# Optimization experiments

Measured on AMD Instinct MI355X. Metric: run time of the kernel, lower is better.

The kernel has to match this reference:

```python
import jax, jax.numpy as jnp
import numpy as np

SIGMA = 0.1  # kernel-point influence radius (KPConv linear correlation)


def setup_inputs() -> dict:
    key = jax.random.key(0)
    k1, k2, k3, k4, k5 = jax.random.split(key, 5)
    N, K, KP, CIN, COUT = 65536, 32, 15, 64, 128
    pos = jax.random.uniform(k1, (N, 3), dtype=jnp.float32)
    feats = jax.random.normal(k2, (N, CIN), dtype=jnp.float32)
    kernel_points = jax.random.normal(k3, (KP, 3), dtype=jnp.float32) * 0.05
    weights = jax.random.normal(k4, (KP, CIN, COUT), dtype=jnp.float32) / np.sqrt(KP * CIN)
    neighbors = jax.random.randint(k5, (N, K), 0, N, dtype=jnp.int64)
    return {"pos": pos, "feats": feats, "kernel_points": kernel_points,
            "weights": weights, "neighbors": neighbors}


def reference(pos, feats, kernel_points, weights, neighbors):
    # pos: [N,3], feats: [N,Cin], kernel_points: [Kp,3],
    # weights: [Kp,Cin,Cout], neighbors: [N,K] int
    neigh_pos = pos[neighbors]                      # [N,K,3] irregular gather
    rel = neigh_pos - pos[:, None, :]               # [N,K,3]
    # distance from each relative neighbor offset to each kernel point
    d = rel[:, :, None, :] - kernel_points[None, None, :, :]   # [N,K,Kp,3]
    dist = jnp.sqrt(jnp.sum(d * d, axis=-1))        # [N,K,Kp]
    infl = jnp.maximum(0.0, 1.0 - dist / SIGMA)     # linear correlation
    neigh_feat = feats[neighbors]                   # [N,K,Cin] irregular gather
    # per-kernel-point weighted neighbor aggregation, then projection
    weighted = jnp.einsum('njk,njc->nkc', infl, neigh_feat)    # [N,Kp,Cin]
    out = jnp.einsum('nkc,kcd->nd', weighted, weights)         # [N,Cout]
    return out
```

## Files before the change

### kernel.cpp

```cpp
#include <hip/hip_runtime.h>

#define NPTS  65536
#define KNB   32
#define KPn   15
#define CIN   64
#define COUT  128
#define MPTS  16
#define THREADS 512
#define RCAP  96
#define CHUNK 32
#define ESTR  40
#define WSTR  1032
#define KSTEPS 32
#define NTILE 8
#define WELEMS (NTILE * KSTEPS * 64 * 8)

#define OFF_INFL   0
#define OFF_SFT    20480
#define ZERO_B16   ((20480 + 5120) / 16)
#define OFF_RLX    25600
#define OFF_RLY    (OFF_RLX + 384)
#define OFF_RLZ    (OFF_RLY + 384)
#define OFF_RLD    (OFF_RLZ + 384)
#define OFF_RSL    (OFF_RLD + 384)
#define POOL_BYTES (MPTS * WSTR * 2)

typedef __attribute__((ext_vector_type(8))) short short8;
typedef __attribute__((ext_vector_type(4))) float f32x4;

__device__ __forceinline__ unsigned int f2bf(float f) {
    union { float f; unsigned int i; } v; v.f = f;
    return (v.i + 0x7fffu + ((v.i >> 16) & 1u)) >> 16;
}
__device__ __forceinline__ unsigned int cvt_pk_bf16(float lo, float hi) {
    unsigned int r;
    asm volatile("v_cvt_pk_bf16_f32 %0, %1, %2" : "=v"(r) : "v"(lo), "v"(hi));
    return r;
}

__global__ void wtrans_kernel(const float* __restrict__ w,
                              const float* __restrict__ kpts,
                              unsigned short* __restrict__ wTf,
                              float4* __restrict__ kpq_out) {
    const int d = blockIdx.x * 256 + threadIdx.x;
    if (d < WELEMS) {
        const int j    = d & 7;
        const int lane = (d >> 3) & 63;
        const int ks   = (d >> 9) & 31;
        const int t    = d >> 14;
        const int f    = ks * 32 + ((lane >> 4) & 3) * 8 + j;
        const int k    = f & 15;
        const int c    = f >> 4;
        const int n    = t * 16 + (lane & 15);
        wTf[d] = (k < KPn)
            ? (unsigned short)f2bf(w[((size_t)k * CIN + c) * COUT + n])
            : (unsigned short)0;
    }
    if (blockIdx.x == 0 && threadIdx.x < 16) {
        const int k = threadIdx.x;
        if (k < KPn) {
            const float x = kpts[k * 3 + 0];
            const float y = kpts[k * 3 + 1];
            const float z = kpts[k * 3 + 2];
            kpq_out[k] = make_float4(x, y, z, x * x + y * y + z * z);
        } else {
            float mx = 0.f;
            for (int i = 0; i < KPn; ++i) {
                const float x = kpts[i * 3 + 0];
                const float y = kpts[i * 3 + 1];
                const float z = kpts[i * 3 + 2];
                mx = fmaxf(mx, x * x + y * y + z * z);
            }
            const float R = 0.1f + sqrtf(mx);
            kpq_out[15] = make_float4(R * R, 0.f, 0.f, 0.f);
        }
    }
}

__global__ __launch_bounds__(THREADS, 8) void kpconv_kernel(
    const float* __restrict__ pos,
    const float* __restrict__ feats,
    const unsigned short* __restrict__ wTf,
    const float4* __restrict__ kpq_in,
    const int*   __restrict__ neighbors,
    float*       __restrict__ out)
{
    __shared__ __align__(16) unsigned char pool[POOL_BYTES];
    __shared__ float  cposf[MPTS * 3];
    __shared__ float4 kpq[KPn];
    __shared__ int    nact;

    unsigned short* const wl     = (unsigned short*)pool;
    unsigned short* const infl   = (unsigned short*)(pool + OFF_INFL);
    unsigned short* const sfeatT = (unsigned short*)(pool + OFF_SFT);
    float*          const rlx    = (float*)(pool + OFF_RLX);
    float*          const rly    = (float*)(pool + OFF_RLY);
    float*          const rlz    = (float*)(pool + OFF_RLZ);
    float*          const rld    = (float*)(pool + OFF_RLD);
    unsigned int*   const rsl    = (unsigned int*)(pool + OFF_RSL);

    const int tid  = threadIdx.x;
    const int n0   = blockIdx.x * MPTS;
    const int lane = tid & 63;
    const int wv   = tid >> 6;
    const int m    = lane & 15;
    const int q    = lane >> 4;

    const int   p0  = tid >> 5;
    const int   nb0 = neighbors[(size_t)n0 * KNB + tid];
    const float qx  = pos[(size_t)nb0 * 3 + 0];
    const float qy  = pos[(size_t)nb0 * 3 + 1];
    const float qz  = pos[(size_t)nb0 * 3 + 2];
    const float R2  = kpq_in[15].x;

    if (tid < KPn) kpq[tid] = kpq_in[tid];
    if (tid == 0) nact = 0;
    if (tid < MPTS * 3) cposf[tid] = pos[(size_t)n0 * 3 + tid];
    __syncthreads();

    {
        const float rx = qx - cposf[p0 * 3 + 0];
        const float ry = qy - cposf[p0 * 3 + 1];
        const float rz = qz - cposf[p0 * 3 + 2];
        const float d2r = rx * rx + ry * ry + rz * rz;
        if (d2r < R2) {
            const int idx = atomicAdd(&nact, 1);
            if (idx < RCAP) {
                rlx[idx] = rx; rly[idx] = ry; rlz[idx] = rz; rld[idx] = d2r;
                rsl[idx] = ((unsigned int)p0 << 16) | (unsigned int)nb0;
            }
        }
    }
    __syncthreads();

    const int E   = min(nact, RCAP);
    const int nch = (E + CHUNK - 1) >> 5;

    f32x4 acc[2][4];
    #pragma unroll
    for (int i = 0; i < 2; ++i)
        #pragma unroll
        for (int nt = 0; nt < 4; ++nt)
            acc[i][nt] = (f32x4){0.f, 0.f, 0.f, 0.f};

    for (int ch = 0; ch < nch; ++ch) {
        {
            uint4* zp = (uint4*)pool;
            #pragma unroll
            for (int i = 0; i < 4; ++i) {
                const int idx = tid + i * THREADS;
                if (idx < ZERO_B16) zp[idx] = make_uint4(0u, 0u, 0u, 0u);
            }
        }
        __syncthreads();

        const int ce = min(E - ch * CHUNK, CHUNK);

        {
            const int el = tid & 31;
            const int c4 = tid >> 5;
            if (el < ce) {
                const int nb = (int)(rsl[ch * CHUNK + el] & 0xFFFFu);
                const float4 f = *(const float4*)(feats + (size_t)nb * CIN + c4 * 4);
                sfeatT[(c4 * 4 + 0) * ESTR + el] = (unsigned short)f2bf(f.x);
                sfeatT[(c4 * 4 + 1) * ESTR + el] = (unsigned short)f2bf(f.y);
                sfeatT[(c4 * 4 + 2) * ESTR + el] = (unsigned short)f2bf(f.z);
                sfeatT[(c4 * 4 + 3) * ESTR + el] = (unsigned short)f2bf(f.w);
            }
        }
        if (tid < ce * 16) {
            const int el = tid >> 4;
            const int k  = tid & 15;
            if (k < KPn) {
                const int e = ch * CHUNK + el;
                const float4 kp  = kpq[k];
                const float  d2r = rld[e];
                const float dot = rlx[e] * kp.x + rly[e] * kp.y + rlz[e] * kp.z;
                if (dot > 0.5f * (d2r - 0.01f + kp.w)) {
                    const float d2 = fmaxf(d2r - 2.f * dot + kp.w, 0.f);
                    const float w  = 1.0f - 10.0f * sqrtf(d2);
                    const int p = (int)(rsl[e] >> 16);
                    infl[(p * 16 + k) * ESTR + el] = (unsigned short)f2bf(w);
                }
            }
        }
        __syncthreads();

        {
            const short8 aA = *(const short8*)(infl + ((wv * 2 + 0) * 16 + m) * ESTR + q * 8);
            const short8 aB = *(const short8*)(infl + ((wv * 2 + 1) * 16 + m) * ESTR + q * 8);
            #pragma unroll
            for (int nt = 0; nt < 4; ++nt) {
                const short8 b = *(const short8*)(sfeatT + (nt * 16 + m) * ESTR + q * 8);
                acc[0][nt] = __builtin_amdgcn_mfma_f32_16x16x32_bf16(aA, b, acc[0][nt], 0, 0, 0);
                acc[1][nt] = __builtin_amdgcn_mfma_f32_16x16x32_bf16(aB, b, acc[1][nt], 0, 0, 0);
            }
        }
        __syncthreads();
    }

    #pragma unroll
    for (int i = 0; i < 2; ++i) {
        const int p = wv * 2 + i;
        #pragma unroll
        for (int nt = 0; nt < 4; ++nt) {
            const int c = nt * 16 + m;
            unsigned short* wp = wl + p * WSTR + c * 16 + q * 4;
            *(unsigned int*)(wp)     = cvt_pk_bf16(acc[i][nt][0], acc[i][nt][1]);
            *(unsigned int*)(wp + 2) = cvt_pk_bf16(acc[i][nt][2], acc[i][nt][3]);
        }
    }
    __syncthreads();

    {
        f32x4 o = {0.f, 0.f, 0.f, 0.f};
        const unsigned short* ap = wl + m * WSTR + q * 8;
        const short8* bp = (const short8*)wTf + (size_t)wv * KSTEPS * 64 + lane;

        #pragma unroll 4
        for (int ks = 0; ks < KSTEPS; ++ks, ap += 32) {
            const short8 a = *(const short8*)ap;
            const short8 b = bp[ks * 64];
            o = __builtin_amdgcn_mfma_f32_16x16x32_bf16(a, b, o, 0, 0, 0);
        }

        const int c = wv * 16 + m;
        #pragma unroll
        for (int r = 0; r < 4; ++r)
            out[(size_t)(n0 + q * 4 + r) * COUT + c] = o[r];
    }
}

extern "C" void kernel_launch(void* const* d_in, const int* in_sizes, int n_in,
                              void* d_out, int out_size, void* d_ws, size_t ws_size,
                              hipStream_t stream) {
    const float* pos       = (const float*)d_in[0];
    const float* feats     = (const float*)d_in[1];
    const float* kpts      = (const float*)d_in[2];
    const float* weights   = (const float*)d_in[3];
    const int*   neighbors = (const int*)d_in[4];
    float*       out       = (float*)d_out;
    unsigned short* wTf    = (unsigned short*)d_ws;
    float4* kpq            = (float4*)((char*)d_ws + WELEMS * 2);

    wtrans_kernel<<<WELEMS / 256, 256, 0, stream>>>(weights, kpts, wTf, kpq);
    kpconv_kernel<<<NPTS / MPTS, THREADS, 0, stream>>>(
        pos, feats, wTf, kpq, neighbors, out);
}
```

Before: 146.1 us.

## Split neighbor aggregation into two passes over point halves to shrink scratch

The influence-times-feature aggregation now runs in two passes, each covering 8 of the 16 center points. Each wave keeps one accumulator set instead of two, and the influence scratch shrinks to 128 rows so it fits in the output pool after the weighted buffer. The relative-position arrays move out of the pool into their own shared arrays, and feature staging now writes zeros for inactive slots. The aim is fewer registers and less zeroing per chunk, at the cost of gathering features and running the chunk loop twice.

```diff
diff --git a/kernel.cpp b/kernel.cpp
--- a/kernel.cpp
+++ b/kernel.cpp
@@ -15,15 +15,10 @@
 #define NTILE 8
 #define WELEMS (NTILE * KSTEPS * 64 * 8)
 
-#define OFF_INFL   0
-#define OFF_SFT    20480
-#define ZERO_B16   ((20480 + 5120) / 16)
-#define OFF_RLX    25600
-#define OFF_RLY    (OFF_RLX + 384)
-#define OFF_RLZ    (OFF_RLY + 384)
-#define OFF_RLD    (OFF_RLZ + 384)
-#define OFF_RSL    (OFF_RLD + 384)
 #define POOL_BYTES (MPTS * WSTR * 2)
+#define OFF_SCR    16512
+#define OFF_SFT    (OFF_SCR + 128 * ESTR * 2)
+#define ZINFL_B16  (128 * ESTR * 2 / 16)
 
 typedef __attribute__((ext_vector_type(8))) short short8;
 typedef __attribute__((ext_vector_type(4))) float f32x4;
@@ -88,16 +83,13 @@
     __shared__ __align__(16) unsigned char pool[POOL_BYTES];
     __shared__ float  cposf[MPTS * 3];
     __shared__ float4 kpq[KPn];
+    __shared__ float  rlx[RCAP], rly[RCAP], rlz[RCAP], rld[RCAP];
+    __shared__ unsigned int rsl[RCAP];
     __shared__ int    nact;
 
-    unsigned short* const wl     = (unsigned short*)pool;
-    unsigned short* const infl   = (unsigned short*)(pool + OFF_INFL);
-    unsigned short* const sfeatT = (unsigned short*)(pool + OFF_SFT);
-    float*          const rlx    = (float*)(pool + OFF_RLX);
-    float*          const rly    = (float*)(pool + OFF_RLY);
-    float*          const rlz    = (float*)(pool + OFF_RLZ);
-    float*          const rld    = (float*)(pool + OFF_RLD);
-    unsigned int*   const rsl    = (unsigned int*)(pool + OFF_RSL);
+    unsigned short* const wl   = (unsigned short*)pool;
+    unsigned short* const infl = (unsigned short*)(pool + OFF_SCR);
+    unsigned short* const sfT  = (unsigned short*)(pool + OFF_SFT);
 
     const int tid  = threadIdx.x;
     const int n0   = blockIdx.x * MPTS;
@@ -136,78 +128,76 @@
     const int E   = min(nact, RCAP);
     const int nch = (E + CHUNK - 1) >> 5;
 
-    f32x4 acc[2][4];
-    #pragma unroll
-    for (int i = 0; i < 2; ++i)
+    for (int pass = 0; pass < 2; ++pass) {
+        f32x4 acc[4];
         #pragma unroll
-        for (int nt = 0; nt < 4; ++nt)
-            acc[i][nt] = (f32x4){0.f, 0.f, 0.f, 0.f};
-
-    for (int ch = 0; ch < nch; ++ch) {
+        for (int nt = 0; nt < 4; ++nt) acc[nt] = (f32x4){0.f, 0.f, 0.f, 0.f};
+
+        for (int ch = 0; ch < nch; ++ch) {
+            const int ce = min(E - ch * CHUNK, CHUNK);
+
+            {
+                uint4* zp = (uint4*)infl;
+                #pragma unroll
+                for (int i = 0; i < 2; ++i) {
+                    const int idx = tid + i * THREADS;
+                    if (idx < ZINFL_B16) zp[idx] = make_uint4(0u, 0u, 0u, 0u);
+                }
+                const int el = tid & 31;
+                const int c4 = tid >> 5;
+                float4 f = make_float4(0.f, 0.f, 0.f, 0.f);
+                if (el < ce) {
+                    const int nb = (int)(rsl[ch * CHUNK + el] & 0xFFFFu);
+                    f = *(const float4*)(feats + (size_t)nb * CIN + c4 * 4);
+                }
+                sfT[(c4 * 4 + 0) * ESTR + el] = (unsigned short)f2bf(f.x);
+                sfT[(c4 * 4 + 1) * ESTR + el] = (unsigned short)f2bf(f.y);
+                sfT[(c4 * 4 + 2) * ESTR + el] = (unsigned short)f2bf(f.z);
+                sfT[(c4 * 4 + 3) * ESTR + el] = (unsigned short)f2bf(f.w);
+            }
+            __syncthreads();
+
+            if (tid < ce * 16) {
+                const int el = tid >> 4;
+                const int k  = tid & 15;
+                if (k < KPn) {
+                    const int e = ch * CHUNK + el;
+                    const int p = (int)(rsl[e] >> 16);
+                    if ((p >> 3) == pass) {
+                        const float4 kp  = kpq[k];
+                        const float  d2r = rld[e];
+                        const float dot = rlx[e]*kp.x + rly[e]*kp.y + rlz[e]*kp.z;
+                        if (dot > 0.5f * (d2r - 0.01f + kp.w)) {
+                            const float d2 = fmaxf(d2r - 2.f * dot + kp.w, 0.f);
+                            const float w  = 1.0f - 10.0f * sqrtf(d2);
+                            infl[((p & 7) * 16 + k) * ESTR + el] =
+                                (unsigned short)f2bf(w);
+                        }
+                    }
+                }
+            }
+            __syncthreads();
+
+            {
+                const short8 a = *(const short8*)(infl + (wv * 16 + m) * ESTR + q * 8);
+                #pragma unroll
+                for (int nt = 0; nt < 4; ++nt) {
+                    const short8 b = *(const short8*)(sfT + (nt * 16 + m) * ESTR + q * 8);
+                    acc[nt] = __builtin_amdgcn_mfma_f32_16x16x32_bf16(a, b, acc[nt], 0, 0, 0);
+                }
+            }
+            __syncthreads();
+        }
+
         {
-            uint4* zp = (uint4*)pool;
-            #pragma unroll
-            for (int i = 0; i < 4; ++i) {
-                const int idx = tid + i * THREADS;
-                if (idx < ZERO_B16) zp[idx] = make_uint4(0u, 0u, 0u, 0u);
-            }
-        }
-        __syncthreads();
-
-        const int ce = min(E - ch * CHUNK, CHUNK);
-
-        {
-            const int el = tid & 31;
-            const int c4 = tid >> 5;
-            if (el < ce) {
-                const int nb = (int)(rsl[ch * CHUNK + el] & 0xFFFFu);
-                const float4 f = *(const float4*)(feats + (size_t)nb * CIN + c4 * 4);
-                sfeatT[(c4 * 4 + 0) * ESTR + el] = (unsigned short)f2bf(f.x);
-                sfeatT[(c4 * 4 + 1) * ESTR + el] = (unsigned short)f2bf(f.y);
-                sfeatT[(c4 * 4 + 2) * ESTR + el] = (unsigned short)f2bf(f.z);
-                sfeatT[(c4 * 4 + 3) * ESTR + el] = (unsigned short)f2bf(f.w);
-            }
-        }
-        if (tid < ce * 16) {
-            const int el = tid >> 4;
-            const int k  = tid & 15;
-            if (k < KPn) {
-                const int e = ch * CHUNK + el;
-                const float4 kp  = kpq[k];
-                const float  d2r = rld[e];
-                const float dot = rlx[e] * kp.x + rly[e] * kp.y + rlz[e] * kp.z;
-                if (dot > 0.5f * (d2r - 0.01f + kp.w)) {
-                    const float d2 = fmaxf(d2r - 2.f * dot + kp.w, 0.f);
-                    const float w  = 1.0f - 10.0f * sqrtf(d2);
-                    const int p = (int)(rsl[e] >> 16);
-                    infl[(p * 16 + k) * ESTR + el] = (unsigned short)f2bf(w);
-                }
-            }
-        }
-        __syncthreads();
-
-        {
-            const short8 aA = *(const short8*)(infl + ((wv * 2 + 0) * 16 + m) * ESTR + q * 8);
-            const short8 aB = *(const short8*)(infl + ((wv * 2 + 1) * 16 + m) * ESTR + q * 8);
+            const int prow = pass * 8 + wv;
             #pragma unroll
             for (int nt = 0; nt < 4; ++nt) {
-                const short8 b = *(const short8*)(sfeatT + (nt * 16 + m) * ESTR + q * 8);
-                acc[0][nt] = __builtin_amdgcn_mfma_f32_16x16x32_bf16(aA, b, acc[0][nt], 0, 0, 0);
-                acc[1][nt] = __builtin_amdgcn_mfma_f32_16x16x32_bf16(aB, b, acc[1][nt], 0, 0, 0);
-            }
-        }
-        __syncthreads();
-    }
-
-    #pragma unroll
-    for (int i = 0; i < 2; ++i) {
-        const int p = wv * 2 + i;
-        #pragma unroll
-        for (int nt = 0; nt < 4; ++nt) {
-            const int c = nt * 16 + m;
-            unsigned short* wp = wl + p * WSTR + c * 16 + q * 4;
-            *(unsigned int*)(wp)     = cvt_pk_bf16(acc[i][nt][0], acc[i][nt][1]);
-            *(unsigned int*)(wp + 2) = cvt_pk_bf16(acc[i][nt][2], acc[i][nt][3]);
+                const int c = nt * 16 + m;
+                unsigned short* wp = wl + prow * WSTR + c * 16 + q * 4;
+                *(unsigned int*)(wp)     = cvt_pk_bf16(acc[nt][0], acc[nt][1]);
+                *(unsigned int*)(wp + 2) = cvt_pk_bf16(acc[nt][2], acc[nt][3]);
+            }
         }
     }
     __syncthreads();
```

New measurement: 136.0 us. -6.9%, faster.
